# Optimization experiments

Measured on AMD Instinct MI355X. Metric: run time of the kernel, lower is better.

Reference implementation:

```python
import jax, jax.numpy as jnp
import numpy as np

B, N, C_IN = 8, 8192, 64
M, K, RADIUS = 1024, 64, 0.2
MLP = [64, 64, 128]


def _fps(pts, m):
    """Iterative farthest point sampling. pts: [N,3] -> [m] int32 indices."""
    n = pts.shape[0]

    def step(carry, _):
        dists, last = carry
        d = jnp.sum((pts - pts[last]) ** 2, axis=-1)          # [N]
        dists = jnp.minimum(dists, d)
        nxt = jnp.argmax(dists).astype(jnp.int32)
        return (dists, nxt), nxt

    init = (jnp.full((n,), 1e10, pts.dtype), jnp.int32(0))
    _, idx = jax.lax.scan(step, init, None, length=m - 1)
    return jnp.concatenate([jnp.zeros((1,), jnp.int32), idx])


def _ball_query(new_xyz, xyz, radius, k):
    """new_xyz: [B,3,M], xyz: [B,3,N] -> [B,M,K] neighbor indices.
    First k points within radius (in index order); padded with first hit."""
    d2 = (jnp.sum(new_xyz ** 2, 1)[:, :, None] + jnp.sum(xyz ** 2, 1)[:, None, :]
          - 2.0 * jnp.einsum('bcm,bcn->bmn', new_xyz, xyz))   # [B,M,N]
    mask = d2 < radius * radius
    # stable argsort of ~mask puts indices of in-radius points first, in order
    order = jnp.argsort(jnp.where(mask, 0, 1).astype(jnp.int32), axis=-1)[..., :k]
    count = jnp.sum(mask, axis=-1)                             # [B,M]
    valid = jnp.arange(k)[None, None, :] < count[..., None]
    return jnp.where(valid, order, order[..., :1])


def _group(x, idx):
    """x: [B,C,N], idx: [B,...] -> [B,C,...] gathered along N."""
    return jax.vmap(lambda a, i: a[:, i])(x, idx)


def _forward(xyz, feature, params):
    # FPS centroid indices (torch runs under no_grad -> stop_gradient)
    pts = jax.lax.stop_gradient(jnp.transpose(xyz, (0, 2, 1)))  # [B,N,3]
    cidx = jax.vmap(lambda p: _fps(p, M))(pts)                  # [B,M]
    new_xyz = _group(xyz, cidx)                                 # [B,3,M]
    nidx = _ball_query(jax.lax.stop_gradient(new_xyz),
                       jax.lax.stop_gradient(xyz), RADIUS, K)   # [B,M,K]
    gxyz = _group(xyz, nidx) - new_xyz[..., None]               # [B,3,M,K]
    x = jnp.concatenate([gxyz, _group(feature, nidx)], axis=1)  # [B,3+C,M,K]
    # SharedMLP: 1x1 conv2d + BN (folded to per-channel scale/bias) + ReLU
    for w, s, b in params:
        x = jax.nn.relu(jnp.einsum('oi,bimk->bomk', w, x)
                        * s[:, None, None] + b[:, None, None])
    return new_xyz, jnp.max(x, axis=3)                          # [B,3,M], [B,128,M]


def setup_inputs() -> dict:
    key = jax.random.key(0)
    ks = jax.random.split(key, 5)
    inp = {
        'xyz': jax.random.normal(ks[0], (B, 3, N), jnp.float32),
        'feature': jax.random.normal(ks[1], (B, C_IN, N), jnp.float32),
    }
    prev = C_IN + 3  # use_xyz=True
    for li, co in enumerate(MLP):
        inp[f'w{li}'] = jax.random.normal(ks[2 + li], (co, prev), jnp.float32) / np.sqrt(prev).astype(np.float32)
        inp[f's{li}'] = jnp.ones((co,), jnp.float32)
        inp[f'b{li}'] = jnp.zeros((co,), jnp.float32)
        prev = co
    return inp


def reference(xyz, feature, w0, s0, b0, w1, s1, b1, w2, s2, b2):
    return _forward(xyz, feature, ((w0, s0, b0), (w1, s1, b1), (w2, s2, b2)))
```

## Files before the change

kernel.cpp:

```cpp
#include <hip/hip_runtime.h>


#define B_ 8
#define N_ 8192
#define M_ 1024
#define K_ 64
#define FTW 68

template <int CTRL>
__device__ __forceinline__ unsigned long long dpp_key(unsigned long long k) {
  int lo = __builtin_amdgcn_update_dpp(0, (int)(unsigned int)k, CTRL, 0xF, 0xF, true);
  int hi = __builtin_amdgcn_update_dpp(0, (int)(unsigned int)(k >> 32), CTRL, 0xF, 0xF, true);
  unsigned long long o = ((unsigned long long)(unsigned int)hi << 32) | (unsigned int)lo;
  return o > k ? o : k;
}

template <int CTRL>
__device__ __forceinline__ float dpp_fmax(float v) {
  int o = __builtin_amdgcn_update_dpp(0, __float_as_int(v), CTRL, 0xF, 0xF, true);
  return fmaxf(v, __int_as_float(o));
}
__device__ __forceinline__ float wave_fmax63(float v) {
  v = dpp_fmax<0xB1>(v);
  v = dpp_fmax<0x4E>(v);
  v = dpp_fmax<0x141>(v);
  v = dpp_fmax<0x140>(v);
  v = dpp_fmax<0x142>(v);
  v = dpp_fmax<0x143>(v);
  return v;
}

__global__ __launch_bounds__(256, 1) void fps_ft_kernel(const float* __restrict__ xyz,
                                                        const float* __restrict__ feat,
                                                        const float* __restrict__ w0,
                                                        float* __restrict__ w0pad,
                                                        float* __restrict__ ft,
                                                        float* __restrict__ nxyz) {
#pragma clang fp contract(off)
  if (blockIdx.x >= 8) {
    if (blockIdx.x == 8) {
      for (int i = threadIdx.x; i < 64 * FTW; i += 256) {
        int o = i / FTW, c = i % FTW;
        w0pad[i] = (c < 67) ? w0[o * 67 + c] : 0.f;
      }
    }
    const int nb = gridDim.x - 8;
    const int total = B_ * N_ * FTW;
    for (int idx = (blockIdx.x - 8) * 256 + threadIdx.x; idx < total; idx += nb * 256) {
      int c = idx % FTW;
      int bn = idx / FTW;
      int n = bn & (N_ - 1);
      int b = bn >> 13;
      float v;
      if (c < 3) v = xyz[(b * 3 + c) * N_ + n];
      else if (c < 67) v = feat[(b * 64 + (c - 3)) * N_ + n];
      else v = 0.f;
      ft[idx] = v;
    }
    return;
  }

  __shared__ float4 pts4[N_];
  __shared__ unsigned long long cand[2][16];
  __shared__ int scidx[M_];
  const int b = blockIdx.x;
  const int t = threadIdx.x;
  const int lane = t & 63;
  const int wid = t >> 6;
  const float* xb = xyz + b * 3 * N_;

  for (int n = t; n < N_; n += 256) {
    pts4[n] = make_float4(xb[n], xb[N_ + n], xb[2 * N_ + n], 0.f);
  }

  const int base = t * 32;
  float px[32], py[32], pz[32], mind[32];
#pragma unroll
  for (int j = 0; j < 32; ++j) {
    px[j] = xb[base + j];
    py[j] = xb[N_ + base + j];
    pz[j] = xb[2 * N_ + base + j];
    mind[j] = 1e10f;
  }
  float xl = xb[0], yl = xb[N_], zl = xb[2 * N_];
  if (t == 0) scidx[0] = 0;
  __syncthreads();

  for (int i = 1; i < M_; ++i) {
    float bestv = -1.f;
    int bl = 0;
#pragma unroll
    for (int j = 0; j < 32; ++j) {
      float dx = __fsub_rn(px[j], xl);
      float dy = __fsub_rn(py[j], yl);
      float dz = __fsub_rn(pz[j], zl);
      float d = __fadd_rn(__fadd_rn(__fmul_rn(dx, dx), __fmul_rn(dy, dy)), __fmul_rn(dz, dz));
      float md = fminf(mind[j], d);
      mind[j] = md;
      if (md > bestv) { bestv = md; bl = j; }
    }
    unsigned long long key =
        ((unsigned long long)__float_as_uint(bestv) << 32) | (unsigned int)(~(base + bl));
    key = dpp_key<0xB1>(key);
    key = dpp_key<0x4E>(key);
    key = dpp_key<0x141>(key);
    key = dpp_key<0x140>(key);
    if ((lane & 15) == 0) cand[i & 1][wid * 4 + (lane >> 4)] = key;
    __syncthreads();
    unsigned long long gk = cand[i & 1][lane & 15];
    gk = dpp_key<0xB1>(gk);
    gk = dpp_key<0x4E>(gk);
    gk = dpp_key<0x141>(gk);
    gk = dpp_key<0x140>(gk);
    const int gi = (int)(~(unsigned int)gk);
    if (t == 0) scidx[i] = gi;
    float4 cc = pts4[gi];
    xl = cc.x; yl = cc.y; zl = cc.z;
  }
  __syncthreads();
  for (int q = t; q < M_; q += 256) {
    int ci = scidx[q];
    float4 c = pts4[ci];
    nxyz[b * 3 * M_ + q] = c.x;
    nxyz[b * 3 * M_ + M_ + q] = c.y;
    nxyz[b * 3 * M_ + 2 * M_ + q] = c.z;
  }
}

__global__ __launch_bounds__(256) void ballq_kernel(const float* __restrict__ xyz,
                                                    const float* __restrict__ nxyz,
                                                    int* __restrict__ nidx) {
  const int lane = threadIdx.x & 63;
  const int g = blockIdx.x * 4 + (threadIdx.x >> 6);
  const int b = g >> 10;
  const int m = g & (M_ - 1);
  const float* xb = xyz + b * 3 * N_;
  const float cx = nxyz[b * 3 * M_ + m];
  const float cy = nxyz[b * 3 * M_ + M_ + m];
  const float cz = nxyz[b * 3 * M_ + 2 * M_ + m];
  const float nc = __fadd_rn(__fadd_rn(__fmul_rn(cx, cx), __fmul_rn(cy, cy)), __fmul_rn(cz, cz));
  int cnt = 0;
  int first = 0;
  int* slot = nidx + (g << 6);
  for (int basei = 0; basei < N_ && cnt < K_; basei += 64) {
    const int n = basei + lane;
    float p_x = xb[n], p_y = xb[N_ + n], p_z = xb[2 * N_ + n];
    float pn = __fadd_rn(__fadd_rn(__fmul_rn(p_x, p_x), __fmul_rn(p_y, p_y)), __fmul_rn(p_z, p_z));
    float dt = __fadd_rn(__fadd_rn(__fmul_rn(cx, p_x), __fmul_rn(cy, p_y)), __fmul_rn(cz, p_z));
    float d2 = __fsub_rn(__fadd_rn(nc, pn), __fmul_rn(2.f, dt));
    bool inr = d2 < 0.04f;
    unsigned long long mk = __ballot(inr);
    if (cnt == 0 && mk != 0ull) first = basei + (__ffsll((long long)mk) - 1);
    int pos = cnt + (int)__popcll(mk & ((1ull << lane) - 1ull));
    if (inr && pos < K_) slot[pos] = n;
    cnt += (int)__popcll(mk);
  }
  if (cnt > K_) cnt = K_;
  if (lane >= cnt) slot[lane] = first;
}

__global__ __launch_bounds__(64, 3) void mlp_t_kernel(
    const float* __restrict__ ft, const float* __restrict__ w0pad,
    const int* __restrict__ nidx, const float* __restrict__ nxyz,
    const float* __restrict__ s0, const float* __restrict__ b0,
    const float* __restrict__ w1, const float* __restrict__ s1, const float* __restrict__ b1,
    const float* __restrict__ w2, const float* __restrict__ s2, const float* __restrict__ b2,
    float* __restrict__ out2) {
  __shared__ float xls[64 * FTW];
  const int g = blockIdx.x;
  const int b = g >> 10;
  const int m = g & (M_ - 1);
  const int lane = threadIdx.x;

  const float cx = nxyz[b * 3 * M_ + m];
  const float cy = nxyz[b * 3 * M_ + M_ + m];
  const float cz = nxyz[b * 3 * M_ + 2 * M_ + m];

  {
    const int nk = nidx[(g << 6) + lane];
    const float4* src = (const float4*)(ft + (size_t)((b << 13) + nk) * FTW);
    float4* dst = (float4*)(xls + lane * FTW);
    float4 v0 = src[0];
    v0.x -= cx; v0.y -= cy; v0.z -= cz;
    dst[0] = v0;
#pragma unroll
    for (int q = 1; q < 17; ++q) dst[q] = src[q];
  }

  float w0r[FTW];
  {
    const float4* wp = (const float4*)(w0pad + lane * FTW);
#pragma unroll
    for (int q = 0; q < 17; ++q) {
      float4 wv = wp[q];
      w0r[4 * q + 0] = wv.x; w0r[4 * q + 1] = wv.y;
      w0r[4 * q + 2] = wv.z; w0r[4 * q + 3] = wv.w;
    }
  }
  const float s0l = s0[lane], b0l = b0[lane];
  for (int k = 0; k < 64; k += 2) {
    const float4* rowA = (const float4*)(xls + k * FTW);
    const float4* rowB = (const float4*)(xls + (k + 1) * FTW);
    float aA = 0.f, aB = 0.f;
#pragma unroll
    for (int q = 0; q < 17; ++q) {
      float4 xa = rowA[q];
      float4 xbv = rowB[q];
      aA = fmaf(w0r[4 * q + 0], xa.x, aA);
      aA = fmaf(w0r[4 * q + 1], xa.y, aA);
      aA = fmaf(w0r[4 * q + 2], xa.z, aA);
      aA = fmaf(w0r[4 * q + 3], xa.w, aA);
      aB = fmaf(w0r[4 * q + 0], xbv.x, aB);
      aB = fmaf(w0r[4 * q + 1], xbv.y, aB);
      aB = fmaf(w0r[4 * q + 2], xbv.z, aB);
      aB = fmaf(w0r[4 * q + 3], xbv.w, aB);
    }
    xls[k * FTW + lane] = fmaxf(fmaf(aA, s0l, b0l), 0.f);
    xls[(k + 1) * FTW + lane] = fmaxf(fmaf(aB, s0l, b0l), 0.f);
  }

  float w1r[64];
  {
    const float4* wp = (const float4*)(w1 + lane * 64);
#pragma unroll
    for (int q = 0; q < 16; ++q) {
      float4 wv = wp[q];
      w1r[4 * q + 0] = wv.x; w1r[4 * q + 1] = wv.y;
      w1r[4 * q + 2] = wv.z; w1r[4 * q + 3] = wv.w;
    }
  }
  const float s1l = s1[lane], b1l = b1[lane];
  for (int k = 0; k < 64; k += 2) {
    const float4* rowA = (const float4*)(xls + k * FTW);
    const float4* rowB = (const float4*)(xls + (k + 1) * FTW);
    float aA = 0.f, aB = 0.f;
#pragma unroll
    for (int q = 0; q < 16; ++q) {
      float4 xa = rowA[q];
      float4 xbv = rowB[q];
      aA = fmaf(w1r[4 * q + 0], xa.x, aA);
      aA = fmaf(w1r[4 * q + 1], xa.y, aA);
      aA = fmaf(w1r[4 * q + 2], xa.z, aA);
      aA = fmaf(w1r[4 * q + 3], xa.w, aA);
      aB = fmaf(w1r[4 * q + 0], xbv.x, aB);
      aB = fmaf(w1r[4 * q + 1], xbv.y, aB);
      aB = fmaf(w1r[4 * q + 2], xbv.z, aB);
      aB = fmaf(w1r[4 * q + 3], xbv.w, aB);
    }
    xls[k * FTW + lane] = fmaxf(fmaf(aA, s1l, b1l), 0.f);
    xls[(k + 1) * FTW + lane] = fmaxf(fmaf(aB, s1l, b1l), 0.f);
  }

  float w2a[64], w2b[64];
  {
    const float4* wpa = (const float4*)(w2 + lane * 64);
    const float4* wpb = (const float4*)(w2 + (64 + lane) * 64);
#pragma unroll
    for (int q = 0; q < 16; ++q) {
      float4 wv = wpa[q];
      w2a[4 * q + 0] = wv.x; w2a[4 * q + 1] = wv.y;
      w2a[4 * q + 2] = wv.z; w2a[4 * q + 3] = wv.w;
      float4 wu = wpb[q];
      w2b[4 * q + 0] = wu.x; w2b[4 * q + 1] = wu.y;
      w2b[4 * q + 2] = wu.z; w2b[4 * q + 3] = wu.w;
    }
  }
  const float s2a = s2[lane], b2a = b2[lane];
  const float s2b = s2[64 + lane], b2b = b2[64 + lane];
  float vmaxA = 0.f, vmaxB = 0.f;
  for (int k = 0; k < 64; ++k) {
    const float4* row = (const float4*)(xls + k * FTW);
    float aA = 0.f, aB = 0.f;
#pragma unroll
    for (int q = 0; q < 16; ++q) {
      float4 xa = row[q];
      aA = fmaf(w2a[4 * q + 0], xa.x, aA);
      aA = fmaf(w2a[4 * q + 1], xa.y, aA);
      aA = fmaf(w2a[4 * q + 2], xa.z, aA);
      aA = fmaf(w2a[4 * q + 3], xa.w, aA);
      aB = fmaf(w2b[4 * q + 0], xa.x, aB);
      aB = fmaf(w2b[4 * q + 1], xa.y, aB);
      aB = fmaf(w2b[4 * q + 2], xa.z, aB);
      aB = fmaf(w2b[4 * q + 3], xa.w, aB);
    }
    vmaxA = fmaxf(vmaxA, fmaxf(fmaf(aA, s2a, b2a), 0.f));
    vmaxB = fmaxf(vmaxB, fmaxf(fmaf(aB, s2b, b2b), 0.f));
  }
  out2[(size_t)((b << 7) + lane) * M_ + m] = vmaxA;
  out2[(size_t)((b << 7) + 64 + lane) * M_ + m] = vmaxB;
}

__global__ __launch_bounds__(64, 4) void mlp_kernel_fb(
    const float* __restrict__ xyz, const float* __restrict__ feat,
    const int* __restrict__ nidx, const float* __restrict__ nxyz,
    const float* __restrict__ w0, const float* __restrict__ s0, const float* __restrict__ b0,
    const float* __restrict__ w1, const float* __restrict__ s1, const float* __restrict__ b1,
    const float* __restrict__ w2, const float* __restrict__ s2, const float* __restrict__ b2,
    float* __restrict__ out2) {
  __shared__ float ylds[64 * 33];
  const int g = blockIdx.x;
  const int b = g >> 10;
  const int m = g & (M_ - 1);
  const int lane = threadIdx.x;
  const int n = nidx[(g << 6) + lane];
  const float cx = nxyz[b * 3 * M_ + m];
  const float cy = nxyz[b * 3 * M_ + M_ + m];
  const float cz = nxyz[b * 3 * M_ + 2 * M_ + m];

  float x0[67];
  const float* xb = xyz + b * 3 * N_;
  x0[0] = xb[n] - cx; x0[1] = xb[N_ + n] - cy; x0[2] = xb[2 * N_ + n] - cz;
#pragma unroll
  for (int c = 0; c < 64; ++c) x0[3 + c] = feat[((b << 6) + c) * N_ + n];

  float x1[64];
#pragma unroll
  for (int h = 0; h < 2; ++h) {
#pragma unroll 2
    for (int oo = 0; oo < 32; oo += 4) {
      const int o = h * 32 + oo;
      const float* wr = w0 + o * 67;
      float a0 = 0.f, a1 = 0.f, a2 = 0.f, a3 = 0.f;
#pragma unroll
      for (int ci = 0; ci < 67; ++ci) {
        float xvv = x0[ci];
        a0 = fmaf(wr[ci], xvv, a0);
        a1 = fmaf(wr[67 + ci], xvv, a1);
        a2 = fmaf(wr[134 + ci], xvv, a2);
        a3 = fmaf(wr[201 + ci], xvv, a3);
      }
      ylds[lane * 33 + oo + 0] = fmaxf(fmaf(a0, s0[o + 0], b0[o + 0]), 0.f);
      ylds[lane * 33 + oo + 1] = fmaxf(fmaf(a1, s0[o + 1], b0[o + 1]), 0.f);
      ylds[lane * 33 + oo + 2] = fmaxf(fmaf(a2, s0[o + 2], b0[o + 2]), 0.f);
      ylds[lane * 33 + oo + 3] = fmaxf(fmaf(a3, s0[o + 3], b0[o + 3]), 0.f);
    }
#pragma unroll
    for (int c = 0; c < 32; ++c) x1[h * 32 + c] = ylds[lane * 33 + c];
  }

  float x2[64];
#pragma unroll
  for (int h = 0; h < 2; ++h) {
#pragma unroll 2
    for (int oo = 0; oo < 32; oo += 4) {
      const int o = h * 32 + oo;
      const float* wr = w1 + o * 64;
      float a0 = 0.f, a1 = 0.f, a2 = 0.f, a3 = 0.f;
#pragma unroll
      for (int ci = 0; ci < 64; ++ci) {
        float xvv = x1[ci];
        a0 = fmaf(wr[ci], xvv, a0);
        a1 = fmaf(wr[64 + ci], xvv, a1);
        a2 = fmaf(wr[128 + ci], xvv, a2);
        a3 = fmaf(wr[192 + ci], xvv, a3);
      }
      ylds[lane * 33 + oo + 0] = fmaxf(fmaf(a0, s1[o + 0], b1[o + 0]), 0.f);
      ylds[lane * 33 + oo + 1] = fmaxf(fmaf(a1, s1[o + 1], b1[o + 1]), 0.f);
      ylds[lane * 33 + oo + 2] = fmaxf(fmaf(a2, s1[o + 2], b1[o + 2]), 0.f);
      ylds[lane * 33 + oo + 3] = fmaxf(fmaf(a3, s1[o + 3], b1[o + 3]), 0.f);
    }
#pragma unroll
    for (int c = 0; c < 32; ++c) x2[h * 32 + c] = ylds[lane * 33 + c];
  }

  float* outbm = out2 + (size_t)(b * 128) * M_ + m;
#pragma unroll 2
  for (int o = 0; o < 128; o += 4) {
    const float* wr = w2 + o * 64;
    float a0 = 0.f, a1 = 0.f, a2 = 0.f, a3 = 0.f;
#pragma unroll
    for (int ci = 0; ci < 64; ++ci) {
      float xvv = x2[ci];
      a0 = fmaf(wr[ci], xvv, a0);
      a1 = fmaf(wr[64 + ci], xvv, a1);
      a2 = fmaf(wr[128 + ci], xvv, a2);
      a3 = fmaf(wr[192 + ci], xvv, a3);
    }
    float v0 = fmaxf(fmaf(a0, s2[o + 0], b2[o + 0]), 0.f);
    float v1 = fmaxf(fmaf(a1, s2[o + 1], b2[o + 1]), 0.f);
    float v2 = fmaxf(fmaf(a2, s2[o + 2], b2[o + 2]), 0.f);
    float v3 = fmaxf(fmaf(a3, s2[o + 3], b2[o + 3]), 0.f);
    v0 = wave_fmax63(v0);
    v1 = wave_fmax63(v1);
    v2 = wave_fmax63(v2);
    v3 = wave_fmax63(v3);
    float g0 = __int_as_float(__builtin_amdgcn_readlane(__float_as_int(v0), 63));
    float g1 = __int_as_float(__builtin_amdgcn_readlane(__float_as_int(v1), 63));
    float g2 = __int_as_float(__builtin_amdgcn_readlane(__float_as_int(v2), 63));
    float g3 = __int_as_float(__builtin_amdgcn_readlane(__float_as_int(v3), 63));
    if (lane == ((o + 0) & 63)) outbm[(o + 0) * M_] = g0;
    if (lane == ((o + 1) & 63)) outbm[(o + 1) * M_] = g1;
    if (lane == ((o + 2) & 63)) outbm[(o + 2) * M_] = g2;
    if (lane == ((o + 3) & 63)) outbm[(o + 3) * M_] = g3;
  }
}

extern "C" void kernel_launch(void* const* d_in, const int* in_sizes, int n_in,
                              void* d_out, int out_size, void* d_ws, size_t ws_size,
                              hipStream_t stream) {
  const float* xyz = (const float*)d_in[0];
  const float* feat = (const float*)d_in[1];
  const float* w0 = (const float*)d_in[2];
  const float* s0 = (const float*)d_in[3];
  const float* b0 = (const float*)d_in[4];
  const float* w1 = (const float*)d_in[5];
  const float* s1 = (const float*)d_in[6];
  const float* b1 = (const float*)d_in[7];
  const float* w2 = (const float*)d_in[8];
  const float* s2 = (const float*)d_in[9];
  const float* b2 = (const float*)d_in[10];

  float* nxyz = (float*)d_out;
  float* out2 = (float*)d_out + B_ * 3 * M_;

  const size_t nidx_bytes = (size_t)B_ * M_ * K_ * sizeof(int);
  const size_t w0p_bytes = (size_t)64 * FTW * sizeof(float);
  const size_t ft_bytes = (size_t)B_ * N_ * FTW * sizeof(float);
  int* nidx = (int*)d_ws;
  float* w0pad = (float*)((char*)d_ws + nidx_bytes);
  float* ft = (float*)((char*)d_ws + nidx_bytes + w0p_bytes);
  const bool use_ft = ws_size >= nidx_bytes + w0p_bytes + ft_bytes;

  hipLaunchKernelGGL(fps_ft_kernel, dim3(use_ft ? 64 : 8), dim3(256), 0, stream,
                     xyz, feat, w0, w0pad, ft, nxyz);
  hipLaunchKernelGGL(ballq_kernel, dim3(B_ * M_ / 4), dim3(256), 0, stream, xyz, nxyz, nidx);
  if (use_ft) {
    hipLaunchKernelGGL(mlp_t_kernel, dim3(B_ * M_), dim3(64), 0, stream,
                       ft, w0pad, nidx, nxyz, s0, b0, w1, s1, b1, w2, s2, b2, out2);
  } else {
    hipLaunchKernelGGL(mlp_kernel_fb, dim3(B_ * M_), dim3(64), 0, stream,
                       xyz, feat, nidx, nxyz, w0, s0, b0, w1, s1, b1, w2, s2, b2, out2);
  }
}
```

Baseline: 1.253 ms.

## Split MLP block across two waves each handling half the neighbor rows

The per-centroid MLP kernel now runs 128 threads (two wavefronts), each wave processing 32 of the 64 neighbor rows through all three layers. The gather is also split across thread pairs, and the final max-pool is combined via a small shared-memory reduction. This roughly doubles parallelism per centroid and shortens per-block latency, but adds barriers and duplicates the per-wave weight loads into registers, with launch bounds relaxed to 2 blocks per SIMD occupancy hint.

```diff
diff --git a/kernel.cpp b/kernel.cpp
--- a/kernel.cpp
+++ b/kernel.cpp
@@ -159,7 +159,7 @@
   if (lane >= cnt) slot[lane] = first;
 }
 
-__global__ __launch_bounds__(64, 3) void mlp_t_kernel(
+__global__ __launch_bounds__(128, 2) void mlp_t_kernel(
     const float* __restrict__ ft, const float* __restrict__ w0pad,
     const int* __restrict__ nidx, const float* __restrict__ nxyz,
     const float* __restrict__ s0, const float* __restrict__ b0,
@@ -167,25 +167,37 @@
     const float* __restrict__ w2, const float* __restrict__ s2, const float* __restrict__ b2,
     float* __restrict__ out2) {
   __shared__ float xls[64 * FTW];
+  __shared__ float red[2][128];
   const int g = blockIdx.x;
   const int b = g >> 10;
   const int m = g & (M_ - 1);
-  const int lane = threadIdx.x;
+  const int t = threadIdx.x;
+  const int lane = t & 63;
+  const int wid = t >> 6;
+  const int r0 = wid * 32;
 
   const float cx = nxyz[b * 3 * M_ + m];
   const float cy = nxyz[b * 3 * M_ + M_ + m];
   const float cz = nxyz[b * 3 * M_ + 2 * M_ + m];
 
   {
-    const int nk = nidx[(g << 6) + lane];
+    const int row = t >> 1;
+    const int half = t & 1;
+    const int nk = nidx[(g << 6) + row];
     const float4* src = (const float4*)(ft + (size_t)((b << 13) + nk) * FTW);
-    float4* dst = (float4*)(xls + lane * FTW);
-    float4 v0 = src[0];
-    v0.x -= cx; v0.y -= cy; v0.z -= cz;
-    dst[0] = v0;
-#pragma unroll
-    for (int q = 1; q < 17; ++q) dst[q] = src[q];
-  }
+    float4* dst = (float4*)(xls + row * FTW);
+    if (half == 0) {
+      float4 v0 = src[0];
+      v0.x -= cx; v0.y -= cy; v0.z -= cz;
+      dst[0] = v0;
+#pragma unroll
+      for (int q = 1; q < 8; ++q) dst[q] = src[q];
+    } else {
+#pragma unroll
+      for (int q = 8; q < 17; ++q) dst[q] = src[q];
+    }
+  }
+  __syncthreads();
 
   float w0r[FTW];
   {
@@ -198,7 +210,8 @@
     }
   }
   const float s0l = s0[lane], b0l = b0[lane];
-  for (int k = 0; k < 64; k += 2) {
+  for (int kk = 0; kk < 32; kk += 2) {
+    const int k = r0 + kk;
     const float4* rowA = (const float4*)(xls + k * FTW);
     const float4* rowB = (const float4*)(xls + (k + 1) * FTW);
     float aA = 0.f, aB = 0.f;
@@ -230,7 +243,8 @@
     }
   }
   const float s1l = s1[lane], b1l = b1[lane];
-  for (int k = 0; k < 64; k += 2) {
+  for (int kk = 0; kk < 32; kk += 2) {
+    const int k = r0 + kk;
     const float4* rowA = (const float4*)(xls + k * FTW);
     const float4* rowB = (const float4*)(xls + (k + 1) * FTW);
     float aA = 0.f, aB = 0.f;
@@ -268,8 +282,8 @@
   const float s2a = s2[lane], b2a = b2[lane];
   const float s2b = s2[64 + lane], b2b = b2[64 + lane];
   float vmaxA = 0.f, vmaxB = 0.f;
-  for (int k = 0; k < 64; ++k) {
-    const float4* row = (const float4*)(xls + k * FTW);
+  for (int kk = 0; kk < 32; ++kk) {
+    const float4* row = (const float4*)(xls + (r0 + kk) * FTW);
     float aA = 0.f, aB = 0.f;
 #pragma unroll
     for (int q = 0; q < 16; ++q) {
@@ -286,8 +300,13 @@
     vmaxA = fmaxf(vmaxA, fmaxf(fmaf(aA, s2a, b2a), 0.f));
     vmaxB = fmaxf(vmaxB, fmaxf(fmaf(aB, s2b, b2b), 0.f));
   }
-  out2[(size_t)((b << 7) + lane) * M_ + m] = vmaxA;
-  out2[(size_t)((b << 7) + 64 + lane) * M_ + m] = vmaxB;
+  red[wid][lane] = vmaxA;
+  red[wid][64 + lane] = vmaxB;
+  __syncthreads();
+  if (t < 128) {
+    float v = fmaxf(red[0][t], red[1][t]);
+    out2[(size_t)((b << 7) + t) * M_ + m] = v;
+  }
 }
 
 __global__ __launch_bounds__(64, 4) void mlp_kernel_fb(
@@ -425,7 +444,7 @@
                      xyz, feat, w0, w0pad, ft, nxyz);
   hipLaunchKernelGGL(ballq_kernel, dim3(B_ * M_ / 4), dim3(256), 0, stream, xyz, nxyz, nidx);
   if (use_ft) {
-    hipLaunchKernelGGL(mlp_t_kernel, dim3(B_ * M_), dim3(64), 0, stream,
+    hipLaunchKernelGGL(mlp_t_kernel, dim3(B_ * M_), dim3(128), 0, stream,
                        ft, w0pad, nidx, nxyz, s0, b0, w1, s1, b1, w2, s2, b2, out2);
   } else {
     hipLaunchKernelGGL(mlp_kernel_fb, dim3(B_ * M_), dim3(64), 0, stream,
```

Result: faster. 1.223 ms (-2.4%).
